# Performance work log

Hardware: AMD Instinct MI355X
Metric: run time of the kernel (lower is better)

## Reference

```python
import jax, jax.numpy as jnp
import numpy as np

GROUP_NORM_EPSILON = 1e-06
NUM_GROUPS = 32


def group_norm(x, gamma, beta, num_groups, eps):
    # x: [B, H, W, C]; normalize over (H, W, C//G) within each group.
    B, H, W, C = x.shape
    xg = x.reshape(B, H, W, num_groups, C // num_groups)
    mean = jnp.mean(xg, axis=(1, 2, 4), keepdims=True)
    var = jnp.mean(jnp.square(xg - mean), axis=(1, 2, 4), keepdims=True)
    xn = (xg - mean) * jax.lax.rsqrt(var + eps)
    return xn.reshape(B, H, W, C) * gamma + beta


def setup_inputs() -> dict:
    key = jax.random.key(0)
    ks = jax.random.split(key, 6)
    B, H, W, C = 4, 64, 64, 512
    scale = 1.0 / np.sqrt(C)
    return {
        "inputs": jax.random.normal(ks[0], (B, H, W, C), dtype=jnp.float32),
        "gamma": jnp.ones((C,), dtype=jnp.float32),
        "beta": jnp.zeros((C,), dtype=jnp.float32),
        "Wq": jax.random.normal(ks[1], (C, C), dtype=jnp.float32) * scale,
        "bq": jnp.zeros((C,), dtype=jnp.float32),
        "Wk": jax.random.normal(ks[2], (C, C), dtype=jnp.float32) * scale,
        "bk": jnp.zeros((C,), dtype=jnp.float32),
        "Wv": jax.random.normal(ks[3], (C, C), dtype=jnp.float32) * scale,
        "bv": jnp.zeros((C,), dtype=jnp.float32),
        "Wo": jax.random.normal(ks[4], (C, C), dtype=jnp.float32) * scale,
        "bo": jnp.zeros((C,), dtype=jnp.float32),
    }


def reference(inputs, gamma, beta, Wq, bq, Wk, bk, Wv, bv, Wo, bo):
    B, H, W, C = inputs.shape
    N = H * W
    h = group_norm(inputs, gamma, beta, NUM_GROUPS, GROUP_NORM_EPSILON)
    hf = h.reshape(B, N, C)  # flatten spatial: [B, N, C]
    q = hf @ Wq + bq
    k = hf @ Wk + bk
    v = hf @ Wv + bv
    # full spatial self-attention: [B, N, N]
    scores = jnp.einsum("bnc,bmc->bnm", q, k) * (C ** -0.5)
    attn = jax.nn.softmax(scores, axis=-1)
    out = jnp.einsum("bnm,bmc->bnc", attn, v)
    out = out @ Wo + bo
    return out.reshape(B, H, W, C) + inputs
```

## Files before the change

### kernel.cpp

```cpp
#include <hip/hip_runtime.h>
#include <hip/hip_bf16.h>

using bf16 = __hip_bfloat16;
using u16  = unsigned short;
typedef __attribute__((ext_vector_type(8))) short s16x8;
typedef __attribute__((ext_vector_type(4))) float f32x4;

__device__ __forceinline__ float b2f(u16 u){
  union{unsigned u; float f;} c; c.u = ((unsigned)u)<<16; return c.f;
}
__device__ __forceinline__ u16 f2b(float f){
  union{float f; unsigned u;} c; c.f = f;
  unsigned r = (c.u + 0x7FFFu + ((c.u>>16)&1u)) >> 16;
  return (u16)r;
}

#define GLDS16(g, l_) __builtin_amdgcn_global_load_lds( \
    (const __attribute__((address_space(1))) unsigned int*)(g), \
    (__attribute__((address_space(3))) unsigned int*)(l_), 16, 0, 0)

__global__ __launch_bounds__(512) void gn_kernel(const float* __restrict__ x,
    const float* __restrict__ gamma, const float* __restrict__ beta,
    bf16* __restrict__ h)
{
  const int b = blockIdx.x >> 5, g = blockIdx.x & 31;
  const int t = threadIdx.x;
  const size_t base = (size_t)b*4096*512 + (size_t)g*16;
  float sum = 0.f, sq = 0.f;
  for (int i = 0; i < 8; i++){
    const float* p = x + base + (size_t)(i*512 + t)*512;
    #pragma unroll
    for (int j = 0; j < 4; j++){
      f32x4 v = *(const f32x4*)(p + j*4);
      #pragma unroll
      for (int e = 0; e < 4; e++){ sum += v[e]; sq += v[e]*v[e]; }
    }
  }
  __shared__ float red[16];
  for (int o = 32; o > 0; o >>= 1){ sum += __shfl_xor(sum, o); sq += __shfl_xor(sq, o); }
  const int w = t >> 6, l = t & 63;
  if (l == 0){ red[w] = sum; red[8 + w] = sq; }
  __syncthreads();
  if (t == 0){
    float a = 0.f, bb = 0.f;
    for (int i = 0; i < 8; i++){ a += red[i]; bb += red[8 + i]; }
    red[0] = a; red[8] = bb;
  }
  __syncthreads();
  const float inv_n = 1.f/65536.f;
  const float mean = red[0]*inv_n;
  const float var  = red[8]*inv_n - mean*mean;
  const float rstd = rsqrtf(var + 1e-6f);
  float ga[16], be[16];
  #pragma unroll
  for (int j = 0; j < 16; j++){
    ga[j] = gamma[g*16 + j];
    be[j] = beta [g*16 + j];
  }
  u16* hp = (u16*)h;
  for (int i = 0; i < 8; i++){
    const float* p = x + base + (size_t)(i*512 + t)*512;
    u16* q = hp + base + (size_t)(i*512 + t)*512;
    s16x8 o0, o1;
    #pragma unroll
    for (int j = 0; j < 4; j++){
      f32x4 v = *(const f32x4*)(p + j*4);
      #pragma unroll
      for (int e = 0; e < 4; e++){
        int c = j*4 + e;
        u16 r = f2b((v[e] - mean)*rstd*ga[c] + be[c]);
        if (c < 8) o0[c] = (short)r; else o1[c - 8] = (short)r;
      }
    }
    *(s16x8*)q = o0; *(s16x8*)(q + 8) = o1;
  }
}

struct W4 { const float* p[4]; };
__global__ __launch_bounds__(256) void transpose_w4(W4 srcs, bf16* __restrict__ dst)
{
  __shared__ float tile[64][65];
  const float* in = srcs.p[blockIdx.z];
  u16* out = (u16*)dst + (size_t)blockIdx.z*512*512;
  const int tr = blockIdx.y*64, tc = blockIdx.x*64;
  const int t = threadIdx.x;
  #pragma unroll
  for (int i = 0; i < 16; i++){
    int idx = i*256 + t, r = idx >> 6, c = idx & 63;
    tile[r][c] = in[(size_t)(tr + r)*512 + tc + c];
  }
  __syncthreads();
  #pragma unroll
  for (int i = 0; i < 16; i++){
    int idx = i*256 + t, r = idx >> 6, c = idx & 63;
    out[(size_t)(tc + r)*512 + tr + c] = f2b(tile[c][r]);
  }
}

__global__ __launch_bounds__(256) void transpose_v(const u16* __restrict__ qkv,
    bf16* __restrict__ vT)
{
  __shared__ u16 tile[64][72];
  const u16* in = qkv + 1024 + (size_t)blockIdx.z*4096*1536;
  u16* out = (u16*)vT + (size_t)blockIdx.z*512*4096;
  const int tr = blockIdx.y*64, tc = blockIdx.x*64;
  const int t = threadIdx.x;
  #pragma unroll
  for (int i = 0; i < 16; i++){
    int idx = i*256 + t, r = idx >> 6, c = idx & 63;
    tile[r][c] = in[(size_t)(tr + r)*1536 + tc + c];
  }
  __syncthreads();
  #pragma unroll
  for (int i = 0; i < 16; i++){
    int idx = i*256 + t, r = idx >> 6, c = idx & 63;
    out[(size_t)(tc + r)*4096 + tr + c] = tile[c][r];
  }
}

template<int EPI, typename OutT>
__global__ __launch_bounds__(256) void gemm_bt(
    const u16* __restrict__ A, int lda, long sA,
    const u16* __restrict__ Bt, int ldb, long sB,
    OutT* __restrict__ Cmat, int ldc, long sC,
    int K, float scale,
    const float* __restrict__ b0, const float* __restrict__ b1,
    const float* __restrict__ b2, const float* __restrict__ res)
{
  __shared__ u16 As[128*64];
  __shared__ u16 Bs[128*64];
  const int t = threadIdx.x, l = t & 63, w = t >> 6;
  const int wr = w >> 1, wc = w & 1;
  const int m0 = blockIdx.y * 128, n0 = blockIdx.x * 128;
  const u16* Au  = A  + (size_t)blockIdx.z * sA;
  const u16* Btu = Bt + (size_t)blockIdx.z * sB;

  f32x4 acc[4][4];
  #pragma unroll
  for (int m = 0; m < 4; m++)
    #pragma unroll
    for (int n = 0; n < 4; n++) acc[m][n] = (f32x4){0.f,0.f,0.f,0.f};

  const int srow = l >> 3;
  const int scol = ((l & 7) ^ srow) * 8;
  const int xorv = (l & 7) << 4;
  const int nkt = K >> 6;
  for (int kt = 0; kt < nkt; ++kt){
    const int k0 = kt << 6;
    #pragma unroll
    for (int j = 0; j < 4; j++){
      const int chunk = w*4 + j;
      const int row = chunk*8 + srow;
      GLDS16(Au  + (size_t)(m0 + row)*lda + k0 + scol, &As[chunk*512]);
      GLDS16(Btu + (size_t)(n0 + row)*ldb + k0 + scol, &Bs[chunk*512]);
    }
    __syncthreads();
    #pragma unroll
    for (int kk = 0; kk < 2; kk++){
      const int kbyte = (kk*64 + (l >> 4)*16) ^ xorv;
      s16x8 af[4], bff[4];
      #pragma unroll
      for (int m = 0; m < 4; m++)
        af[m]  = *(const s16x8*)((const char*)As + (wr*64 + m*16 + (l & 15))*128 + kbyte);
      #pragma unroll
      for (int n = 0; n < 4; n++)
        bff[n] = *(const s16x8*)((const char*)Bs + (wc*64 + n*16 + (l & 15))*128 + kbyte);
      #pragma unroll
      for (int m = 0; m < 4; m++)
        #pragma unroll
        for (int n = 0; n < 4; n++)
          acc[m][n] = __builtin_amdgcn_mfma_f32_16x16x32_bf16(af[m], bff[n], acc[m][n], 0, 0, 0);
    }
    __syncthreads();
  }
  const int lc = l & 15, lr4 = (l >> 4)*4;
  OutT* Cz = Cmat + (size_t)blockIdx.z * sC;
  #pragma unroll
  for (int n = 0; n < 4; n++){
    const int col = n0 + wc*64 + n*16 + lc;
    float bv = 0.f;
    if (EPI & 8){
      const float* bp = (col < 512) ? b0 : (col < 1024 ? b1 : b2);
      bv = bp[col & 511];
    } else if (EPI & 1){
      bv = b0[col];
    }
    #pragma unroll
    for (int m = 0; m < 4; m++){
      const int rowb = m0 + wr*64 + m*16 + lr4;
      #pragma unroll
      for (int r = 0; r < 4; r++){
        float v = acc[m][n][r];
        if (EPI & 2) v *= scale;
        v += bv;
        const size_t off = (size_t)(rowb + r)*ldc + col;
        if (EPI & 4) v += res[off];
        if constexpr (__is_same(OutT, float)) Cz[off] = v;
        else ((u16*)Cz)[off] = f2b(v);
      }
    }
  }
}

__global__ __launch_bounds__(256) void softmax_kernel(bf16* __restrict__ S)
{
  const int t = threadIdx.x;
  u16* p = (u16*)S + ((size_t)blockIdx.y*4096 + blockIdx.x)*4096;
  float v[16];
  #pragma unroll
  for (int i = 0; i < 2; i++){
    s16x8 x = *(const s16x8*)(p + (size_t)(i*256 + t)*8);
    #pragma unroll
    for (int j = 0; j < 8; j++) v[i*8 + j] = b2f((u16)x[j]);
  }
  float mx = -1e30f;
  #pragma unroll
  for (int j = 0; j < 16; j++) mx = fmaxf(mx, v[j]);
  for (int o = 32; o > 0; o >>= 1) mx = fmaxf(mx, __shfl_xor(mx, o));
  __shared__ float red[8];
  const int w = t >> 6, l = t & 63;
  if (l == 0) red[w] = mx;
  __syncthreads();
  mx = fmaxf(fmaxf(red[0], red[1]), fmaxf(red[2], red[3]));
  float sum = 0.f;
  #pragma unroll
  for (int j = 0; j < 16; j++){ v[j] = __expf(v[j] - mx); sum += v[j]; }
  for (int o = 32; o > 0; o >>= 1) sum += __shfl_xor(sum, o);
  if (l == 0) red[4 + w] = sum;
  __syncthreads();
  const float inv = 1.f/(red[4] + red[5] + red[6] + red[7]);
  #pragma unroll
  for (int i = 0; i < 2; i++){
    s16x8 x;
    #pragma unroll
    for (int j = 0; j < 8; j++) x[j] = (short)f2b(v[i*8 + j]*inv);
    *(s16x8*)(p + (size_t)(i*256 + t)*8) = x;
  }
}

extern "C" void kernel_launch(void* const* d_in, const int* in_sizes, int n_in,
                              void* d_out, int out_size, void* d_ws, size_t ws_size,
                              hipStream_t stream)
{
  (void)in_sizes; (void)n_in; (void)out_size;
  const float* x     = (const float*)d_in[0];
  const float* gamma = (const float*)d_in[1];
  const float* beta  = (const float*)d_in[2];
  const float* Wq = (const float*)d_in[3]; const float* bq = (const float*)d_in[4];
  const float* Wk = (const float*)d_in[5]; const float* bk = (const float*)d_in[6];
  const float* Wv = (const float*)d_in[7]; const float* bv = (const float*)d_in[8];
  const float* Wo = (const float*)d_in[9]; const float* bo = (const float*)d_in[10];
  float* out = (float*)d_out;

  const int B = 4, N = 4096, C = 512;
  const long NC = (long)N*C;
  const float scl = 0.04419417382415922f;

  char* p0 = (char*)d_ws;
  auto align = [](size_t b){ return (b + 255) & ~(size_t)255; };
  const size_t sz_h   = align((size_t)B*NC*2);
  const size_t sz_w   = align((size_t)4*C*C*2);
  const size_t sz_qkvF= align((size_t)B*N*1536*2);
  const size_t sz_vTF = align((size_t)B*NC*2);
  const size_t sz_aoF = align((size_t)B*NC*2);
  const size_t sz_SF  = align((size_t)B*N*N*2);
  const size_t need_full = sz_h + sz_w + sz_qkvF + sz_vTF + sz_aoF + sz_SF;

  bf16* h    = (bf16*)p0;
  bf16* wAll = (bf16*)(p0 + sz_h);
  char* pv   = p0 + sz_h + sz_w;

  gn_kernel<<<dim3(B*32), dim3(512), 0, stream>>>(x, gamma, beta, h);
  W4 ws4; ws4.p[0] = Wq; ws4.p[1] = Wk; ws4.p[2] = Wv; ws4.p[3] = Wo;
  transpose_w4<<<dim3(8, 8, 4), 256, 0, stream>>>(ws4, wAll);
  bf16* woT = wAll + (size_t)3*C*C;

  if (ws_size >= need_full){
    bf16* qkv = (bf16*)pv;
    bf16* vT  = (bf16*)(pv + sz_qkvF);
    bf16* ao  = (bf16*)(pv + sz_qkvF + sz_vTF);
    bf16* S   = (bf16*)(pv + sz_qkvF + sz_vTF + sz_aoF);

    gemm_bt<8, bf16><<<dim3(12, 128, 1), 256, 0, stream>>>(
        (const u16*)h, C, 0, (const u16*)wAll, C, 0, qkv, 1536, 0,
        C, 1.f, bq, bk, bv, nullptr);
    transpose_v<<<dim3(8, 64, B), 256, 0, stream>>>((const u16*)qkv, vT);
    gemm_bt<2, bf16><<<dim3(32, 32, B), 256, 0, stream>>>(
        (const u16*)qkv, 1536, (long)N*1536, (const u16*)qkv + 512, 1536, (long)N*1536,
        S, N, (long)N*N, C, scl, nullptr, nullptr, nullptr, nullptr);
    softmax_kernel<<<dim3(N, B), 256, 0, stream>>>(S);
    gemm_bt<0, bf16><<<dim3(4, 32, B), 256, 0, stream>>>(
        (const u16*)S, N, (long)N*N, (const u16*)vT, N, NC,
        ao, C, NC, N, 1.f, nullptr, nullptr, nullptr, nullptr);
    gemm_bt<5, float><<<dim3(4, 128, 1), 256, 0, stream>>>(
        (const u16*)ao, C, 0, (const u16*)woT, C, 0, out, C, 0,
        C, 1.f, bo, nullptr, nullptr, x);
  } else {
    const size_t sz_qkv1 = align((size_t)N*1536*2);
    const size_t sz_vT1  = align((size_t)NC*2);
    const size_t sz_ao1  = align((size_t)NC*2);
    bf16* qkv = (bf16*)pv;
    bf16* vT  = (bf16*)(pv + sz_qkv1);
    bf16* ao  = (bf16*)(pv + sz_qkv1 + sz_vT1);
    bf16* S   = (bf16*)(pv + sz_qkv1 + sz_vT1 + sz_ao1);
    for (int b = 0; b < B; b++){
      const u16* hb = (const u16*)h + (size_t)b*NC;
      gemm_bt<8, bf16><<<dim3(12, 32, 1), 256, 0, stream>>>(
          hb, C, 0, (const u16*)wAll, C, 0, qkv, 1536, 0,
          C, 1.f, bq, bk, bv, nullptr);
      transpose_v<<<dim3(8, 64, 1), 256, 0, stream>>>((const u16*)qkv, vT);
      gemm_bt<2, bf16><<<dim3(32, 32, 1), 256, 0, stream>>>(
          (const u16*)qkv, 1536, 0, (const u16*)qkv + 512, 1536, 0,
          S, N, 0, C, scl, nullptr, nullptr, nullptr, nullptr);
      softmax_kernel<<<dim3(N, 1), 256, 0, stream>>>(S);
      gemm_bt<0, bf16><<<dim3(4, 32, 1), 256, 0, stream>>>(
          (const u16*)S, N, 0, (const u16*)vT, N, 0,
          ao, C, 0, N, 1.f, nullptr, nullptr, nullptr, nullptr);
      gemm_bt<5, float><<<dim3(4, 32, 1), 256, 0, stream>>>(
          (const u16*)ao, C, 0, (const u16*)woT, C, 0, out + (size_t)b*NC, C, 0,
          C, 1.f, bo, nullptr, nullptr, x + (size_t)b*NC);
    }
  }
}
```

Baseline: 451.0 us.

## Fuse online softmax into the PV GEMM and swizzle GEMM block order

Drops the separate softmax pass over the bf16 score matrix. A new fused kernel reads the raw scores, runs an online softmax in exp2 domain, with the log2(e) factor folded into the QK scale, and rescales only when the running max grows by more than 8. It then multiplies by V^T with MFMA. This removes one full read and write of the 4096x4096 score matrix per batch. It also adds an XCD-aware block index remap for the GEMM and the fused kernel to improve L2 locality. The risks are low occupancy from 256 blocks of 512 threads with a large LDS footprint, and serial softmax work inside the MFMA loop.

Measured after the change: 613.1 us. 35.9% more time.

```diff
diff --git a/kernel.cpp b/kernel.cpp
--- a/kernel.cpp
+++ b/kernel.cpp
@@ -131,7 +131,16 @@
   __shared__ u16 Bs[128*64];
   const int t = threadIdx.x, l = t & 63, w = t >> 6;
   const int wr = w >> 1, wc = w & 1;
-  const int m0 = blockIdx.y * 128, n0 = blockIdx.x * 128;
+  int bx = blockIdx.x, by = blockIdx.y;
+  {
+    const int gx = gridDim.x, nb = gx * gridDim.y;
+    if ((nb & 7) == 0){
+      int lin = by*gx + bx;
+      int s = (lin & 7)*(nb >> 3) + (lin >> 3);
+      bx = s % gx; by = s / gx;
+    }
+  }
+  const int m0 = by * 128, n0 = bx * 128;
   const u16* Au  = A  + (size_t)blockIdx.z * sA;
   const u16* Btu = Bt + (size_t)blockIdx.z * sB;
 
@@ -202,39 +211,121 @@
   }
 }
 
-__global__ __launch_bounds__(256) void softmax_kernel(bf16* __restrict__ S)
-{
-  const int t = threadIdx.x;
-  u16* p = (u16*)S + ((size_t)blockIdx.y*4096 + blockIdx.x)*4096;
-  float v[16];
-  #pragma unroll
-  for (int i = 0; i < 2; i++){
-    s16x8 x = *(const s16x8*)(p + (size_t)(i*256 + t)*8);
-    #pragma unroll
-    for (int j = 0; j < 8; j++) v[i*8 + j] = b2f((u16)x[j]);
-  }
-  float mx = -1e30f;
-  #pragma unroll
-  for (int j = 0; j < 16; j++) mx = fmaxf(mx, v[j]);
-  for (int o = 32; o > 0; o >>= 1) mx = fmaxf(mx, __shfl_xor(mx, o));
-  __shared__ float red[8];
-  const int w = t >> 6, l = t & 63;
-  if (l == 0) red[w] = mx;
-  __syncthreads();
-  mx = fmaxf(fmaxf(red[0], red[1]), fmaxf(red[2], red[3]));
-  float sum = 0.f;
-  #pragma unroll
-  for (int j = 0; j < 16; j++){ v[j] = __expf(v[j] - mx); sum += v[j]; }
-  for (int o = 32; o > 0; o >>= 1) sum += __shfl_xor(sum, o);
-  if (l == 0) red[4 + w] = sum;
-  __syncthreads();
-  const float inv = 1.f/(red[4] + red[5] + red[6] + red[7]);
-  #pragma unroll
-  for (int i = 0; i < 2; i++){
-    s16x8 x;
-    #pragma unroll
-    for (int j = 0; j < 8; j++) x[j] = (short)f2b(v[i*8 + j]*inv);
-    *(s16x8*)(p + (size_t)(i*256 + t)*8) = x;
+__global__ __launch_bounds__(512) void pv_fused(
+    const u16* __restrict__ S, const u16* __restrict__ vT,
+    bf16* __restrict__ ao, int batched, int batch0)
+{
+  __shared__ u16 Bs[512*64];
+  __shared__ u16 As[64*64];
+  const int t = threadIdx.x, l = t & 63, w = t >> 6;
+  int batch, mt;
+  if (batched){
+    const int lin = blockIdx.x, xcd = lin & 7, slot = lin >> 3;
+    batch = xcd >> 1; mt = ((xcd & 1) << 5) + slot;
+  } else { batch = batch0; mt = blockIdx.x; }
+  const int m0 = mt * 64;
+  const u16* Sb  = S  + (size_t)batch*4096*4096;
+  const u16* vTb = vT + (size_t)batch*512*4096;
+  u16* aob = (u16*)ao + (size_t)batch*4096*512;
+
+  f32x4 acc[4][4];
+  #pragma unroll
+  for (int m = 0; m < 4; m++)
+    #pragma unroll
+    for (int n = 0; n < 4; n++) acc[m][n] = (f32x4){0.f,0.f,0.f,0.f};
+  float mstat[4], lsum[4];
+  #pragma unroll
+  for (int m = 0; m < 4; m++){ mstat[m] = -1e30f; lsum[m] = 0.f; }
+
+  const int srow = l >> 3;
+  const int scol = ((l & 7) ^ srow) * 8;
+  const int xorv = (l & 7) << 4;
+
+  for (int kt = 0; kt < 64; ++kt){
+    const int k0 = kt << 6;
+    #pragma unroll
+    for (int j = 0; j < 8; j++){
+      const int chunk = j*8 + w;
+      const int row = chunk*8 + srow;
+      GLDS16(vTb + (size_t)row*4096 + k0 + scol, &Bs[chunk*512]);
+    }
+    { const int row = w*8 + srow;
+      GLDS16(Sb + (size_t)(m0 + row)*4096 + k0 + scol, &As[w*512]); }
+    __syncthreads();
+
+    s16x8 pa[4][2];
+    #pragma unroll
+    for (int m = 0; m < 4; m++){
+      float sv[16];
+      float tm = -1e30f;
+      #pragma unroll
+      for (int kk = 0; kk < 2; kk++){
+        s16x8 sf = *(const s16x8*)((const char*)As +
+            (m*16 + (l & 15))*128 + ((kk*64 + (l >> 4)*16) ^ xorv));
+        #pragma unroll
+        for (int j = 0; j < 8; j++){
+          float f = b2f((u16)sf[j]); sv[kk*8 + j] = f; tm = fmaxf(tm, f);
+        }
+      }
+      tm = fmaxf(tm, __shfl_xor(tm, 16));
+      tm = fmaxf(tm, __shfl_xor(tm, 32));
+      if (__ballot(tm - mstat[m] > 8.f) != 0ULL){
+        const float nm = fmaxf(mstat[m], tm);
+        const float ff = exp2f(mstat[m] - nm);
+        lsum[m] *= ff; mstat[m] = nm;
+        #pragma unroll
+        for (int r = 0; r < 4; r++){
+          const float fD = __shfl(ff, (l & 48) | ((l >> 4)*4 + r));
+          #pragma unroll
+          for (int n = 0; n < 4; n++) acc[m][n][r] *= fD;
+        }
+      }
+      float rs = 0.f;
+      u16 pb[16];
+      #pragma unroll
+      for (int j = 0; j < 16; j++){
+        const float pvv = exp2f(sv[j] - mstat[m]);
+        rs += pvv;
+        pb[j] = f2b(pvv);
+      }
+      rs += __shfl_xor(rs, 16); rs += __shfl_xor(rs, 32);
+      lsum[m] += rs;
+      #pragma unroll
+      for (int kk = 0; kk < 2; kk++){
+        s16x8 v;
+        #pragma unroll
+        for (int j = 0; j < 8; j++) v[j] = (short)pb[kk*8 + j];
+        pa[m][kk] = v;
+      }
+    }
+    #pragma unroll
+    for (int kk = 0; kk < 2; kk++){
+      const int kbyte = (kk*64 + (l >> 4)*16) ^ xorv;
+      s16x8 bf4[4];
+      #pragma unroll
+      for (int n = 0; n < 4; n++)
+        bf4[n] = *(const s16x8*)((const char*)Bs + (w*64 + n*16 + (l & 15))*128 + kbyte);
+      #pragma unroll
+      for (int m = 0; m < 4; m++)
+        #pragma unroll
+        for (int n = 0; n < 4; n++)
+          acc[m][n] = __builtin_amdgcn_mfma_f32_16x16x32_bf16(pa[m][kk], bf4[n], acc[m][n], 0, 0, 0);
+    }
+    __syncthreads();
+  }
+  #pragma unroll
+  for (int m = 0; m < 4; m++){
+    const float inv = 1.f / lsum[m];
+    #pragma unroll
+    for (int r = 0; r < 4; r++){
+      const float iD = __shfl(inv, (l & 48) | ((l >> 4)*4 + r));
+      const int row = m0 + m*16 + (l >> 4)*4 + r;
+      #pragma unroll
+      for (int n = 0; n < 4; n++){
+        const int col = w*64 + n*16 + (l & 15);
+        aob[(size_t)row*512 + col] = f2b(acc[m][n][r] * iD);
+      }
+    }
   }
 }
 
@@ -254,7 +345,7 @@
 
   const int B = 4, N = 4096, C = 512;
   const long NC = (long)N*C;
-  const float scl = 0.04419417382415922f;
+  const float scl2 = 0.04419417382415922f * 1.4426950408889634f;
 
   char* p0 = (char*)d_ws;
   auto align = [](size_t b){ return (b + 255) & ~(size_t)255; };
@@ -287,11 +378,9 @@
     transpose_v<<<dim3(8, 64, B), 256, 0, stream>>>((const u16*)qkv, vT);
     gemm_bt<2, bf16><<<dim3(32, 32, B), 256, 0, stream>>>(
         (const u16*)qkv, 1536, (long)N*1536, (const u16*)qkv + 512, 1536, (long)N*1536,
-        S, N, (long)N*N, C, scl, nullptr, nullptr, nullptr, nullptr);
-    softmax_kernel<<<dim3(N, B), 256, 0, stream>>>(S);
-    gemm_bt<0, bf16><<<dim3(4, 32, B), 256, 0, stream>>>(
-        (const u16*)S, N, (long)N*N, (const u16*)vT, N, NC,
-        ao, C, NC, N, 1.f, nullptr, nullptr, nullptr, nullptr);
+        S, N, (long)N*N, C, scl2, nullptr, nullptr, nullptr, nullptr);
+    pv_fused<<<dim3(256), 512, 0, stream>>>(
+        (const u16*)S, (const u16*)vT, ao, 1, 0);
     gemm_bt<5, float><<<dim3(4, 128, 1), 256, 0, stream>>>(
         (const u16*)ao, C, 0, (const u16*)woT, C, 0, out, C, 0,
         C, 1.f, bo, nullptr, nullptr, x);
@@ -311,11 +400,9 @@
       transpose_v<<<dim3(8, 64, 1), 256, 0, stream>>>((const u16*)qkv, vT);
       gemm_bt<2, bf16><<<dim3(32, 32, 1), 256, 0, stream>>>(
           (const u16*)qkv, 1536, 0, (const u16*)qkv + 512, 1536, 0,
-          S, N, 0, C, scl, nullptr, nullptr, nullptr, nullptr);
-      softmax_kernel<<<dim3(N, 1), 256, 0, stream>>>(S);
-      gemm_bt<0, bf16><<<dim3(4, 32, 1), 256, 0, stream>>>(
-          (const u16*)S, N, 0, (const u16*)vT, N, 0,
-          ao, C, 0, N, 1.f, nullptr, nullptr, nullptr, nullptr);
+          S, N, 0, C, scl2, nullptr, nullptr, nullptr, nullptr);
+      pv_fused<<<dim3(64), 512, 0, stream>>>(
+          (const u16*)S, (const u16*)vT, ao, 0, 0);
       gemm_bt<5, float><<<dim3(4, 32, 1), 256, 0, stream>>>(
           (const u16*)ao, C, 0, (const u16*)woT, C, 0, out + (size_t)b*NC, C, 0,
           C, 1.f, bo, nullptr, nullptr, x + (size_t)b*NC);
```
